# Optimization experiments

Measured on AMD Instinct MI355X. Metric: run time of the kernel, lower is better.

The kernel has to match this reference:

```python
import jax, jax.numpy as jnp
import numpy as np

N, E, H = 50000, 800000, 4
IN_C, HID, OUT = 256, 64, 64
NEG_SLOPE = 0.2   # PyG GATConv default leaky_relu slope
EPS_BN = 1e-5
EPS_SM = 1e-16    # PyG softmax denominator eps


def setup_inputs() -> dict:
    key = jax.random.key(0)
    ks = jax.random.split(key, 16)
    inp = {
        "x": jax.random.normal(ks[0], (N, IN_C), jnp.float32),
        "edge_index": jax.random.randint(ks[1], (2, E), 0, N, jnp.int32),
    }
    dims = [(IN_C, HID), (HID, HID), (HID, OUT)]
    j = 2
    for l, (di, do) in enumerate(dims):
        s = 1.0 / np.sqrt(di)
        inp[f"W{l}"] = jax.random.normal(ks[j], (di, H * do), jnp.float32) * s; j += 1
        inp[f"as{l}"] = jax.random.normal(ks[j], (H, do), jnp.float32) * 0.1; j += 1
        inp[f"ad{l}"] = jax.random.normal(ks[j], (H, do), jnp.float32) * 0.1; j += 1
        inp[f"b{l}"] = jnp.zeros((do,), jnp.float32)
    for l in range(2):  # BN after all but the last conv
        inp[f"g{l}"] = jnp.ones((HID,), jnp.float32)
        inp[f"be{l}"] = jnp.zeros((HID,), jnp.float32)
    return inp


def _gat_layer(x, src, dst, W, a_src, a_dst, bias):
    """PyG GATConv, heads=H, concat=False (mean over heads), add_self_loops already in src/dst."""
    n = x.shape[0]
    C = a_src.shape[1]
    h = (x @ W).reshape(n, H, C)                      # [N,H,C]
    a_l = jnp.einsum('nhc,hc->nh', h, a_src)          # src attention term per node
    a_r = jnp.einsum('nhc,hc->nh', h, a_dst)          # dst attention term per node
    e = jax.nn.leaky_relu(a_l[src] + a_r[dst], NEG_SLOPE)   # [E',H]
    # segment softmax over incoming edges of each dst node
    m = jax.ops.segment_max(e, dst, num_segments=n)
    m = jnp.where(jnp.isfinite(m), m, 0.0)
    p = jnp.exp(e - m[dst])
    den = jax.ops.segment_sum(p, dst, num_segments=n)
    alpha = p / (den[dst] + EPS_SM)                   # [E',H]
    msg = h[src] * alpha[:, :, None]                  # [E',H,C]
    out = jax.ops.segment_sum(msg, dst, num_segments=n)
    return out.mean(axis=1) + bias                    # concat=False -> head mean, then bias


def _bn(x, g, b):
    # BatchNorm1d training-mode statistics (biased variance), eps=1e-5
    mu = x.mean(axis=0)
    var = x.var(axis=0)
    return (x - mu) * jax.lax.rsqrt(var + EPS_BN) * g + b


def reference(x, edge_index, W0, as0, ad0, b0, W1, as1, ad1, b1,
              W2, as2, ad2, b2, g0, be0, g1, be1):
    n = x.shape[0]
    loops = jnp.arange(n, dtype=edge_index.dtype)
    src = jnp.concatenate([edge_index[0], loops])
    dst = jnp.concatenate([edge_index[1], loops])

    h = _gat_layer(x, src, dst, W0, as0, ad0, b0)
    h = jax.nn.relu(_bn(h, g0, be0))                  # dropout: eval mode (identity)
    h = _gat_layer(h, src, dst, W1, as1, ad1, b1)
    h = jax.nn.relu(_bn(h, g1, be1))
    out = _gat_layer(h, src, dst, W2, as2, ad2, b2)
    return out
```

## Files before the change

### kernel.cpp

```cpp
#include <hip/hip_runtime.h>
#include <hip/hip_fp16.h>
#include <math.h>

constexpr float NEG_SLOPE = 0.2f;
constexpr float EPS_BN = 1e-5f;
constexpr float EPS_SM = 1e-16f;

typedef _Float16 half8 __attribute__((ext_vector_type(8)));
typedef float f32x4 __attribute__((ext_vector_type(4)));

__device__ __forceinline__ float lrelu(float x){ return x >= 0.f ? x : NEG_SLOPE * x; }

typedef const __attribute__((address_space(1))) unsigned int* gas_u32;
typedef __attribute__((address_space(3))) unsigned int* las_u32;

__device__ __forceinline__ void llds16(const _Float16* g, _Float16* l){
  __builtin_amdgcn_global_load_lds((gas_u32)(const void*)g, (las_u32)(void*)l, 16, 0, 0);
}

__global__ void k_prep1(const float* __restrict__ x, _Float16* __restrict__ xh, int n8,
                        const int* __restrict__ ei, int E, int* __restrict__ cnt,
                        int* __restrict__ rank,
                        const float* __restrict__ W0, const float* __restrict__ W1,
                        const float* __restrict__ W2, _Float16* __restrict__ Wt0,
                        _Float16* __restrict__ Wt1, _Float16* __restrict__ Wt2,
                        float* __restrict__ bn, int* __restrict__ tick){
  int t = blockIdx.x * blockDim.x + threadIdx.x;
  if (t < n8){
    const float4* p = (const float4*)(x + (size_t)t * 8);
    float4 v0 = p[0], v1 = p[1];
    half8 h = {(_Float16)v0.x, (_Float16)v0.y, (_Float16)v0.z, (_Float16)v0.w,
               (_Float16)v1.x, (_Float16)v1.y, (_Float16)v1.z, (_Float16)v1.w};
    *(half8*)(xh + (size_t)t * 8) = h;
  }
  if (t < E) rank[t] = atomicAdd(&cnt[ei[E + t]], 1);
  if (t < 256) bn[t] = 0.f;
  if (t < 4) tick[t] = 0;
  if (t < 65536){
    int c = t & 255, k = t >> 8;
    Wt0[(size_t)c * 256 + k] = (_Float16)W0[(size_t)k * 256 + c];
  } else if (t < 81920){
    int u = t - 65536; int c = u & 255, k = u >> 8;
    Wt1[(size_t)c * 64 + k] = (_Float16)W1[(size_t)k * 256 + c];
  } else if (t < 98304){
    int u = t - 81920; int c = u & 255, k = u >> 8;
    Wt2[(size_t)c * 64 + k] = (_Float16)W2[(size_t)k * 256 + c];
  }
}

__global__ __launch_bounds__(256) void k_bsumscan(const int* __restrict__ cnt, int n, int chunk,
                                                  int* __restrict__ part, int* __restrict__ ptr,
                                                  int* __restrict__ tick){
  __shared__ int s[256];
  __shared__ int amLast;
  int b = blockIdx.x, t = threadIdx.x;
  int lo = b * chunk, hi = min(n, lo + chunk);
  int v = 0;
  for (int i = lo + t; i < hi; i += 256) v += cnt[i] + 1;
  s[t] = v;
  __syncthreads();
  #pragma unroll
  for (int off = 128; off > 0; off >>= 1){
    if (t < off) s[t] += s[t + off];
    __syncthreads();
  }
  if (t == 0) part[b] = s[0];
  __threadfence();
  if (t == 0) amLast = (atomicAdd(tick, 1) == (int)gridDim.x - 1) ? 1 : 0;
  __syncthreads();
  if (amLast){
    int pv = atomicAdd(&part[t], 0);
    s[t] = pv;
    __syncthreads();
    #pragma unroll
    for (int off = 1; off < 256; off <<= 1){
      int u = (t >= off) ? s[t - off] : 0;
      __syncthreads();
      s[t] += u;
      __syncthreads();
    }
    part[t] = s[t] - pv;
    if (t == 255) ptr[n] = s[255];
  }
}

__global__ __launch_bounds__(256) void k_localscan(const int* __restrict__ cnt, const int* __restrict__ part,
                                                   int n, int chunk, int* __restrict__ ptr,
                                                   int* __restrict__ csr_src){
  __shared__ int s[256];
  int b = blockIdx.x, t = threadIdx.x;
  int i = b * chunk + t;
  int c = (t < chunk && i < n) ? cnt[i] : 0;
  int v = (t < chunk && i < n) ? c + 1 : 0;
  s[t] = v;
  __syncthreads();
  #pragma unroll
  for (int off = 1; off < 256; off <<= 1){
    int u = (t >= off) ? s[t - off] : 0;
    __syncthreads();
    s[t] += u;
    __syncthreads();
  }
  if (t < chunk && i < n){
    int ex = part[b] + s[t] - v;
    ptr[i] = ex;
    csr_src[ex + c] = i;
  }
}

template<int LAYER>
__global__ __launch_bounds__(256, 2) void k_gemm(const _Float16* __restrict__ Xh,
    const float* __restrict__ Xf,
    const _Float16* __restrict__ Wt, const float* __restrict__ a_s, const float* __restrict__ a_d,
    __half* __restrict__ hb, float* __restrict__ al, float* __restrict__ ar, int nrows,
    const float* __restrict__ scale, const float* __restrict__ shift,
    const int* __restrict__ ei, int E, const int* __restrict__ rank,
    const int* __restrict__ rowptr, int* __restrict__ csr_src,
    int gemmBlocks, int N){
  constexpr int K = (LAYER == 0) ? 256 : 64;
  if (LAYER == 0 && (int)blockIdx.x >= gemmBlocks){
    int fb = (int)blockIdx.x - gemmBlocks;
    int xcd = (int)blockIdx.x & 7;
    int grp = fb >> 3;
    int ngrp = ((int)gridDim.x - gemmBlocks) >> 3;
    int nPer = N >> 3;
    int lo = xcd * nPer;
    int hi = (xcd == 7) ? N : lo + nPer;
    int stride = ngrp * 256;
    for (int e = grp * 256 + (int)threadIdx.x; e < E; e += stride){
      int dst = ei[E + e];
      if (dst >= lo && dst < hi)
        csr_src[rowptr[dst] + rank[e]] = ei[e];
    }
    return;
  }
  __shared__ _Float16 Alds[4][129][8];
  __shared__ _Float16 Blds[4][257][8];
  int tid = threadIdx.x;
  int m0 = blockIdx.x * 128;
  int w = tid >> 6, l = tid & 63;
  int lm = l & 15, lq = l >> 4;
  f32x4 acc[8][4] = {};

  for (int k0 = 0; k0 < K; k0 += 32){
    if (LAYER == 0){
      #pragma unroll
      for (int it = 0; it < 2; it++){
        int gr = m0 + it * 64 + l;
        if (gr < nrows)
          llds16(Xh + (size_t)gr * K + k0 + w * 8, &Alds[w][it * 64][0]);
      }
    } else {
      float4 sc0 = *(const float4*)(scale + k0 + w * 8);
      float4 sc1 = *(const float4*)(scale + k0 + w * 8 + 4);
      float4 sh0 = *(const float4*)(shift + k0 + w * 8);
      float4 sh1 = *(const float4*)(shift + k0 + w * 8 + 4);
      #pragma unroll
      for (int it = 0; it < 2; it++){
        int row = it * 64 + l;
        int gr = m0 + row;
        float4 v0 = make_float4(0,0,0,0), v1 = make_float4(0,0,0,0);
        if (gr < nrows){
          v0 = *(const float4*)(Xf + (size_t)gr * K + k0 + w * 8);
          v1 = *(const float4*)(Xf + (size_t)gr * K + k0 + w * 8 + 4);
        }
        v0.x = fmaxf(fmaf(v0.x, sc0.x, sh0.x), 0.f);
        v0.y = fmaxf(fmaf(v0.y, sc0.y, sh0.y), 0.f);
        v0.z = fmaxf(fmaf(v0.z, sc0.z, sh0.z), 0.f);
        v0.w = fmaxf(fmaf(v0.w, sc0.w, sh0.w), 0.f);
        v1.x = fmaxf(fmaf(v1.x, sc1.x, sh1.x), 0.f);
        v1.y = fmaxf(fmaf(v1.y, sc1.y, sh1.y), 0.f);
        v1.z = fmaxf(fmaf(v1.z, sc1.z, sh1.z), 0.f);
        v1.w = fmaxf(fmaf(v1.w, sc1.w, sh1.w), 0.f);
        half8 h = {(_Float16)v0.x, (_Float16)v0.y, (_Float16)v0.z, (_Float16)v0.w,
                   (_Float16)v1.x, (_Float16)v1.y, (_Float16)v1.z, (_Float16)v1.w};
        *(half8*)&Alds[w][row][0] = h;
      }
    }
    #pragma unroll
    for (int it = 0; it < 4; it++){
      int col = it * 64 + l;
      llds16(Wt + (size_t)col * K + k0 + w * 8, &Blds[w][it * 64][0]);
    }
    __syncthreads();
    half8 af[8];
    #pragma unroll
    for (int mf = 0; mf < 8; mf++) af[mf] = *(const half8*)&Alds[lq][mf * 16 + lm][0];
    #pragma unroll
    for (int j = 0; j < 4; j++){
      half8 bf = *(const half8*)&Blds[lq][(w * 4 + j) * 16 + lm][0];
      #pragma unroll
      for (int mf = 0; mf < 8; mf++)
        acc[mf][j] = __builtin_amdgcn_mfma_f32_16x16x32_f16(af[mf], bf, acc[mf][j], 0, 0, 0);
    }
    __syncthreads();
  }

  float asv[4], adv[4];
  #pragma unroll
  for (int j = 0; j < 4; j++){
    asv[j] = a_s[w * 64 + j * 16 + lm];
    adv[j] = a_d[w * 64 + j * 16 + lm];
  }
  #pragma unroll
  for (int mf = 0; mf < 8; mf++){
    #pragma unroll
    for (int reg = 0; reg < 4; reg++){
      float sl = acc[mf][0][reg] * asv[0] + acc[mf][1][reg] * asv[1]
               + acc[mf][2][reg] * asv[2] + acc[mf][3][reg] * asv[3];
      float sr = acc[mf][0][reg] * adv[0] + acc[mf][1][reg] * adv[1]
               + acc[mf][2][reg] * adv[2] + acc[mf][3][reg] * adv[3];
      #pragma unroll
      for (int off = 1; off < 16; off <<= 1){
        sl += __shfl_xor(sl, off);
        sr += __shfl_xor(sr, off);
      }
      int row = m0 + mf * 16 + lq * 4 + reg;
      if (lm == 0 && row < nrows){
        al[(size_t)row * 4 + w] = sl;
        ar[(size_t)row * 4 + w] = sr;
      }
      if (row < nrows){
        ushort4 pk;
        pk.x = __half_as_ushort(__float2half(acc[mf][0][reg]));
        pk.y = __half_as_ushort(__float2half(acc[mf][1][reg]));
        pk.z = __half_as_ushort(__float2half(acc[mf][2][reg]));
        pk.w = __half_as_ushort(__float2half(acc[mf][3][reg]));
        *(ushort4*)(hb + (size_t)row * 256 + w * 64 + lm * 4) = pk;
      }
    }
  }
}

#define AGG_STEP(QV, POFF) { \
    int je = j + (POFF) + eh; \
    float w = wbase[je * 4 + hd]; \
    int4 qq = QV; \
    int jn = je + 8; \
    if (jn < deg){ \
      int s = sbase[jn]; \
      QV = *(const int4*)((const char*)hb + (((unsigned)s << 9) + choff)); \
    } \
    const __half2* h2 = (const __half2*)&qq; \
    float2 f0 = __half22float2(h2[0]); \
    float2 f1 = __half22float2(h2[1]); \
    float2 f2 = __half22float2(h2[2]); \
    float2 f3 = __half22float2(h2[3]); \
    a0 = fmaf(f0.x, w, a0); a1 = fmaf(f0.y, w, a1); \
    a2 = fmaf(f1.x, w, a2); a3 = fmaf(f1.y, w, a3); \
    a4 = fmaf(f2.x, w, a4); a5 = fmaf(f2.y, w, a5); \
    a6 = fmaf(f3.x, w, a6); a7 = fmaf(f3.y, w, a7); \
  }

__global__ __launch_bounds__(256, 8) void k_node(const int* __restrict__ ptr,
    const int* __restrict__ csr, const __half* __restrict__ hb,
    const float* __restrict__ al, const float* __restrict__ ar,
    const float* __restrict__ bias, float* __restrict__ out, int N){
  __shared__ float4 wsm[4][64];
  __shared__ int    ssm[4][64];
  int n = (blockIdx.x * blockDim.x + threadIdx.x) >> 6;
  int lane = threadIdx.x & 63;
  int wv = threadIdx.x >> 6;
  if (n >= N) return;
  int beg = ptr[n], end = ptr[n + 1];
  int deg = end - beg;
  float4 arv = *(const float4*)(ar + (size_t)n * 4);

  if (deg <= 64){
    int idx = beg + lane;
    bool act = idx < end;
    int mye = act ? csr[idx] : 0;
    int eh = lane >> 5;
    int hd = (lane >> 3) & 3;
    int c8 = lane & 7;
    unsigned choff = (unsigned)(hd * 128 + c8 * 16);

    float e0 = -1e30f, e1 = -1e30f, e2 = -1e30f, e3 = -1e30f;
    if (act){
      float4 av = *(const float4*)((const char*)al + ((unsigned)mye << 4));
      e0 = lrelu(av.x + arv.x); e1 = lrelu(av.y + arv.y);
      e2 = lrelu(av.z + arv.z); e3 = lrelu(av.w + arv.w);
    }
    int s0 = __shfl(mye, 0 + eh), s1 = __shfl(mye, 2 + eh);
    int s2 = __shfl(mye, 4 + eh), s3 = __shfl(mye, 6 + eh);
    int4 q0 = *(const int4*)((const char*)hb + (((unsigned)s0 << 9) + choff));
    int4 q1 = *(const int4*)((const char*)hb + (((unsigned)s1 << 9) + choff));
    int4 q2 = *(const int4*)((const char*)hb + (((unsigned)s2 << 9) + choff));
    int4 q3 = *(const int4*)((const char*)hb + (((unsigned)s3 << 9) + choff));

    float m0 = e0, m1 = e1, m2 = e2, m3 = e3;
    #pragma unroll
    for (int off = 32; off > 0; off >>= 1){
      m0 = fmaxf(m0, __shfl_xor(m0, off));
      m1 = fmaxf(m1, __shfl_xor(m1, off));
      m2 = fmaxf(m2, __shfl_xor(m2, off));
      m3 = fmaxf(m3, __shfl_xor(m3, off));
    }
    float w0 = __expf(e0 - m0), w1 = __expf(e1 - m1);
    float w2 = __expf(e2 - m2), w3 = __expf(e3 - m3);
    float d0 = w0, d1 = w1, d2 = w2, d3 = w3;
    #pragma unroll
    for (int off = 32; off > 0; off >>= 1){
      d0 += __shfl_xor(d0, off);
      d1 += __shfl_xor(d1, off);
      d2 += __shfl_xor(d2, off);
      d3 += __shfl_xor(d3, off);
    }
    wsm[wv][lane] = make_float4(w0 / (d0 + EPS_SM), w1 / (d1 + EPS_SM),
                                w2 / (d2 + EPS_SM), w3 / (d3 + EPS_SM));
    ssm[wv][lane] = mye;
    __builtin_amdgcn_wave_barrier();

    const float* wbase = (const float*)&wsm[wv][0];
    const int*   sbase = &ssm[wv][0];
    float a0=0.f,a1=0.f,a2=0.f,a3=0.f,a4=0.f,a5=0.f,a6=0.f,a7=0.f;
    for (int j = 0; j < deg; j += 8){
      AGG_STEP(q0, 0)
      AGG_STEP(q1, 2)
      AGG_STEP(q2, 4)
      AGG_STEP(q3, 6)
    }
    #pragma unroll
    for (int off = 32; off >= 8; off >>= 1){
      a0 += __shfl_xor(a0, off); a1 += __shfl_xor(a1, off);
      a2 += __shfl_xor(a2, off); a3 += __shfl_xor(a3, off);
      a4 += __shfl_xor(a4, off); a5 += __shfl_xor(a5, off);
      a6 += __shfl_xor(a6, off); a7 += __shfl_xor(a7, off);
    }
    if (lane < 8){
      float* op = out + (size_t)n * 64 + c8 * 2;
      float2 b0 = *(const float2*)(bias + 0 * 16 + c8 * 2);
      float2 b1 = *(const float2*)(bias + 1 * 16 + c8 * 2);
      float2 b2 = *(const float2*)(bias + 2 * 16 + c8 * 2);
      float2 b3 = *(const float2*)(bias + 3 * 16 + c8 * 2);
      *(float2*)(op + 0)  = make_float2(a0 * 0.25f + b0.x, a4 * 0.25f + b0.y);
      *(float2*)(op + 16) = make_float2(a1 * 0.25f + b1.x, a5 * 0.25f + b1.y);
      *(float2*)(op + 32) = make_float2(a2 * 0.25f + b2.x, a6 * 0.25f + b2.y);
      *(float2*)(op + 48) = make_float2(a3 * 0.25f + b3.x, a7 * 0.25f + b3.y);
    }
  } else {
    int hd = lane >> 4;
    int t = lane & 15;
    const __half* hbase = hb + hd * 64 + t * 4;
    float ax = 0.f, ay = 0.f, az = 0.f, aw = 0.f;
    float m0 = -1e30f, m1 = -1e30f, m2 = -1e30f, m3 = -1e30f;
    for (int i = beg + lane; i < end; i += 64){
      int s = csr[i];
      float4 av = *(const float4*)(al + (size_t)s * 4);
      m0 = fmaxf(m0, lrelu(av.x + arv.x));
      m1 = fmaxf(m1, lrelu(av.y + arv.y));
      m2 = fmaxf(m2, lrelu(av.z + arv.z));
      m3 = fmaxf(m3, lrelu(av.w + arv.w));
    }
    #pragma unroll
    for (int off = 32; off > 0; off >>= 1){
      m0 = fmaxf(m0, __shfl_xor(m0, off));
      m1 = fmaxf(m1, __shfl_xor(m1, off));
      m2 = fmaxf(m2, __shfl_xor(m2, off));
      m3 = fmaxf(m3, __shfl_xor(m3, off));
    }
    float d0 = 0.f, d1 = 0.f, d2 = 0.f, d3 = 0.f;
    for (int i = beg + lane; i < end; i += 64){
      int s = csr[i];
      float4 av = *(const float4*)(al + (size_t)s * 4);
      d0 += __expf(lrelu(av.x + arv.x) - m0);
      d1 += __expf(lrelu(av.y + arv.y) - m1);
      d2 += __expf(lrelu(av.z + arv.z) - m2);
      d3 += __expf(lrelu(av.w + arv.w) - m3);
    }
    #pragma unroll
    for (int off = 32; off > 0; off >>= 1){
      d0 += __shfl_xor(d0, off);
      d1 += __shfl_xor(d1, off);
      d2 += __shfl_xor(d2, off);
      d3 += __shfl_xor(d3, off);
    }
    float i0 = 1.f / (d0 + EPS_SM), i1 = 1.f / (d1 + EPS_SM);
    float i2 = 1.f / (d2 + EPS_SM), i3 = 1.f / (d3 + EPS_SM);
    float arh = hd == 0 ? arv.x : hd == 1 ? arv.y : hd == 2 ? arv.z : arv.w;
    float mh  = hd == 0 ? m0 : hd == 1 ? m1 : hd == 2 ? m2 : m3;
    float ih  = hd == 0 ? i0 : hd == 1 ? i1 : hd == 2 ? i2 : i3;
    for (int i = beg; i < end; i++){
      int s = csr[i];
      float w = __expf(lrelu(al[(size_t)s * 4 + hd] + arh) - mh) * ih;
      ushort4 u = *(const ushort4*)(hbase + (size_t)s * 256);
      ax = fmaf(__half2float(__ushort_as_half(u.x)), w, ax);
      ay = fmaf(__half2float(__ushort_as_half(u.y)), w, ay);
      az = fmaf(__half2float(__ushort_as_half(u.z)), w, az);
      aw = fmaf(__half2float(__ushort_as_half(u.w)), w, aw);
    }
    #pragma unroll
    for (int off = 16; off <= 32; off <<= 1){
      ax += __shfl_xor(ax, off);
      ay += __shfl_xor(ay, off);
      az += __shfl_xor(az, off);
      aw += __shfl_xor(aw, off);
    }
    if (lane < 16){
      float* op = out + (size_t)n * 64;
      op[t]      = ax * 0.25f + bias[t];
      op[16 + t] = ay * 0.25f + bias[16 + t];
      op[32 + t] = az * 0.25f + bias[32 + t];
      op[48 + t] = aw * 0.25f + bias[48 + t];
    }
  }
}

__global__ __launch_bounds__(256) void k_bnstats(const float* __restrict__ x, int N,
                                                 float* __restrict__ gsum, float* __restrict__ gsq,
                                                 int* __restrict__ tick,
                                                 const float* __restrict__ g, const float* __restrict__ be,
                                                 float* __restrict__ scale, float* __restrict__ shift){
  int c = threadIdx.x & 63;
  int rg = threadIdx.x >> 6;
  float s = 0.f, q = 0.f;
  for (int r = blockIdx.x * 4 + rg; r < N; r += gridDim.x * 4){
    float v = x[(size_t)r * 64 + c];
    s += v; q += v * v;
  }
  __shared__ float ls[4][64], lq[4][64];
  __shared__ int amLast;
  ls[rg][c] = s; lq[rg][c] = q;
  __syncthreads();
  if (rg == 0){
    s = ls[0][c] + ls[1][c] + ls[2][c] + ls[3][c];
    q = lq[0][c] + lq[1][c] + lq[2][c] + lq[3][c];
    atomicAdd(&gsum[c], s);
    atomicAdd(&gsq[c], q);
  }
  __threadfence();
  if (threadIdx.x == 0)
    amLast = (atomicAdd(tick, 1) == (int)gridDim.x - 1) ? 1 : 0;
  __syncthreads();
  if (amLast && threadIdx.x < 64){
    float gs = atomicAdd(&gsum[c], 0.f);
    float gq = atomicAdd(&gsq[c], 0.f);
    float m = gs / (float)N;
    float v = gq / (float)N - m * m;
    float sc = g[c] * rsqrtf(v + EPS_BN);
    scale[c] = sc;
    shift[c] = be[c] - m * sc;
  }
}

extern "C" void kernel_launch(void* const* d_in, const int* in_sizes, int n_in,
                              void* d_out, int out_size, void* d_ws, size_t ws_size,
                              hipStream_t stream){
  const float* x  = (const float*)d_in[0];
  const int*   ei = (const int*)d_in[1];
  const float* W[3]  = {(const float*)d_in[2], (const float*)d_in[6],  (const float*)d_in[10]};
  const float* AS[3] = {(const float*)d_in[3], (const float*)d_in[7],  (const float*)d_in[11]};
  const float* AD[3] = {(const float*)d_in[4], (const float*)d_in[8],  (const float*)d_in[12]};
  const float* BI[3] = {(const float*)d_in[5], (const float*)d_in[9],  (const float*)d_in[13]};
  const float* G[2]  = {(const float*)d_in[14], (const float*)d_in[16]};
  const float* BE[2] = {(const float*)d_in[15], (const float*)d_in[17]};
  const int N = in_sizes[0] / 256;
  const int E = in_sizes[1] / 2;
  const int EN = E + N;

  char* wsb = (char*)d_ws;
  size_t off = 0;
  auto alloc = [&](size_t bytes) -> char* {
    char* p = wsb + off;
    off = (off + bytes + 255) & ~(size_t)255;
    return p;
  };
  int* cnt      = (int*)alloc((size_t)N * 4);
  int* rowptr   = (int*)alloc((size_t)(N + 1) * 4);
  int* part     = (int*)alloc(256 * 4);
  int* rank     = (int*)alloc((size_t)E * 4);
  int* csr      = (int*)alloc((size_t)EN * 4);
  _Float16* xh  = (_Float16*)alloc((size_t)N * 256 * 2);
  _Float16* Wt0 = (_Float16*)alloc((size_t)256 * 256 * 2);
  _Float16* Wt1 = (_Float16*)alloc((size_t)64 * 256 * 2);
  _Float16* Wt2 = (_Float16*)alloc((size_t)64 * 256 * 2);
  __half* hb    = (__half*)alloc((size_t)N * 256 * 2);
  float* al     = (float*)alloc((size_t)N * 4 * 4);
  float* ar     = (float*)alloc((size_t)N * 4 * 4);
  float* bufA   = (float*)alloc((size_t)N * 64 * 4);
  float* bn     = (float*)alloc(256 * 4);
  int*   tick   = (int*)alloc(4 * 4);
  float* murs   = (float*)alloc(128 * 4);

  const int chunk = (N + 255) / 256;
  const int n8 = N * 32;
  const int nodeGrid = (N + 3) / 4;

  hipMemsetAsync(cnt, 0, (size_t)N * 4, stream);
  k_prep1<<<(n8 + 255) / 256, 256, 0, stream>>>(x, xh, n8, ei, E, cnt, rank,
                                                W[0], W[1], W[2], Wt0, Wt1, Wt2, bn, tick);
  k_bsumscan<<<256, 256, 0, stream>>>(cnt, N, chunk, part, rowptr, tick + 2);
  k_localscan<<<256, 256, 0, stream>>>(cnt, part, N, chunk, rowptr, csr);

  int gemmGrid = (N + 127) / 128;
  const int FILLB = 1024;
  k_gemm<0><<<gemmGrid + FILLB, 256, 0, stream>>>(xh, nullptr, Wt0, AS[0], AD[0], hb, al, ar, N,
                                                  nullptr, nullptr, ei, E, rank, rowptr, csr,
                                                  gemmGrid, N);
  k_node<<<nodeGrid, 256, 0, stream>>>(rowptr, csr, hb, al, ar, BI[0], bufA, N);
  k_bnstats<<<256, 256, 0, stream>>>(bufA, N, bn, bn + 64, tick, G[0], BE[0], murs, murs + 64);
  k_gemm<1><<<gemmGrid, 256, 0, stream>>>(nullptr, bufA, Wt1, AS[1], AD[1], hb, al, ar, N,
                                          murs, murs + 64, nullptr, 0, nullptr, nullptr, nullptr,
                                          gemmGrid, N);
  k_node<<<nodeGrid, 256, 0, stream>>>(rowptr, csr, hb, al, ar, BI[1], bufA, N);
  k_bnstats<<<256, 256, 0, stream>>>(bufA, N, bn + 128, bn + 192, tick + 1, G[1], BE[1], murs, murs + 64);
  k_gemm<2><<<gemmGrid, 256, 0, stream>>>(nullptr, bufA, Wt2, AS[2], AD[2], hb, al, ar, N,
                                          murs, murs + 64, nullptr, 0, nullptr, nullptr, nullptr,
                                          gemmGrid, N);
  k_node<<<nodeGrid, 256, 0, stream>>>(rowptr, csr, hb, al, ar, BI[2], (float*)d_out, N);
}
```

Before: 531.6 us.

## Reorder layers 1-2 to aggregate input features before projecting through W

For layers 1 and 2, the linear projection is moved after aggregation: attention logits come from the input features dotted with precomputed W·a vectors. Each head's softmax-weighted sum of 64-wide fp16 inputs is gathered, then one GEMM with a head-stacked, 0.25-scaled weight applies projection, head mean and bias together. This cuts per-edge gather width from 256 to 64 halves per edge per head group and removes the per-layer 256-wide projection of all nodes. The cost is an extra small attention kernel, an N×256 fp16 intermediate, and different fp16 rounding order.

```diff
diff --git a/kernel.cpp b/kernel.cpp
--- a/kernel.cpp
+++ b/kernel.cpp
@@ -23,7 +23,10 @@
                         int* __restrict__ rank,
                         const float* __restrict__ W0, const float* __restrict__ W1,
                         const float* __restrict__ W2, _Float16* __restrict__ Wt0,
-                        _Float16* __restrict__ Wt1, _Float16* __restrict__ Wt2,
+                        _Float16* __restrict__ Wtp1, _Float16* __restrict__ Wtp2,
+                        const float* __restrict__ as1, const float* __restrict__ ad1,
+                        const float* __restrict__ as2, const float* __restrict__ ad2,
+                        float* __restrict__ va,
                         float* __restrict__ bn, int* __restrict__ tick){
   int t = blockIdx.x * blockDim.x + threadIdx.x;
   if (t < n8){
@@ -40,11 +43,24 @@
     int c = t & 255, k = t >> 8;
     Wt0[(size_t)c * 256 + k] = (_Float16)W0[(size_t)k * 256 + c];
   } else if (t < 81920){
-    int u = t - 65536; int c = u & 255, k = u >> 8;
-    Wt1[(size_t)c * 64 + k] = (_Float16)W1[(size_t)k * 256 + c];
+    int u = t - 65536; int c = u & 63, r = u >> 6;
+    Wtp1[(size_t)c * 256 + r] = (_Float16)(0.25f * W1[(size_t)(r & 63) * 256 + (r >> 6) * 64 + c]);
   } else if (t < 98304){
-    int u = t - 81920; int c = u & 255, k = u >> 8;
-    Wt2[(size_t)c * 64 + k] = (_Float16)W2[(size_t)k * 256 + c];
+    int u = t - 81920; int c = u & 63, r = u >> 6;
+    Wtp2[(size_t)c * 256 + r] = (_Float16)(0.25f * W2[(size_t)(r & 63) * 256 + (r >> 6) * 64 + c]);
+  } else if (t < 99328){
+    int u = t - 98304;
+    int layer = u >> 9;
+    int sd = (u >> 8) & 1;
+    int u2 = u & 255;
+    int c = u2 >> 2, h = u2 & 3;
+    const float* Wl = layer ? W2 : W1;
+    const float* av = layer ? (sd ? ad2 : as2) : (sd ? ad1 : as1);
+    float acc = 0.f;
+    #pragma unroll 4
+    for (int k = 0; k < 64; k++)
+      acc += Wl[(size_t)c * 256 + h * 64 + k] * av[h * 64 + k];
+    va[layer * 512 + c * 8 + sd * 4 + h] = acc;
   }
 }
 
@@ -110,14 +126,12 @@
 
 template<int LAYER>
 __global__ __launch_bounds__(256, 2) void k_gemm(const _Float16* __restrict__ Xh,
-    const float* __restrict__ Xf,
     const _Float16* __restrict__ Wt, const float* __restrict__ a_s, const float* __restrict__ a_d,
     __half* __restrict__ hb, float* __restrict__ al, float* __restrict__ ar, int nrows,
-    const float* __restrict__ scale, const float* __restrict__ shift,
     const int* __restrict__ ei, int E, const int* __restrict__ rank,
     const int* __restrict__ rowptr, int* __restrict__ csr_src,
     int gemmBlocks, int N){
-  constexpr int K = (LAYER == 0) ? 256 : 64;
+  constexpr int K = 256;
   if (LAYER == 0 && (int)blockIdx.x >= gemmBlocks){
     int fb = (int)blockIdx.x - gemmBlocks;
     int xcd = (int)blockIdx.x & 7;
@@ -143,39 +157,11 @@
   f32x4 acc[8][4] = {};
 
   for (int k0 = 0; k0 < K; k0 += 32){
-    if (LAYER == 0){
-      #pragma unroll
-      for (int it = 0; it < 2; it++){
-        int gr = m0 + it * 64 + l;
-        if (gr < nrows)
-          llds16(Xh + (size_t)gr * K + k0 + w * 8, &Alds[w][it * 64][0]);
-      }
-    } else {
-      float4 sc0 = *(const float4*)(scale + k0 + w * 8);
-      float4 sc1 = *(const float4*)(scale + k0 + w * 8 + 4);
-      float4 sh0 = *(const float4*)(shift + k0 + w * 8);
-      float4 sh1 = *(const float4*)(shift + k0 + w * 8 + 4);
-      #pragma unroll
-      for (int it = 0; it < 2; it++){
-        int row = it * 64 + l;
-        int gr = m0 + row;
-        float4 v0 = make_float4(0,0,0,0), v1 = make_float4(0,0,0,0);
-        if (gr < nrows){
-          v0 = *(const float4*)(Xf + (size_t)gr * K + k0 + w * 8);
-          v1 = *(const float4*)(Xf + (size_t)gr * K + k0 + w * 8 + 4);
-        }
-        v0.x = fmaxf(fmaf(v0.x, sc0.x, sh0.x), 0.f);
-        v0.y = fmaxf(fmaf(v0.y, sc0.y, sh0.y), 0.f);
-        v0.z = fmaxf(fmaf(v0.z, sc0.z, sh0.z), 0.f);
-        v0.w = fmaxf(fmaf(v0.w, sc0.w, sh0.w), 0.f);
-        v1.x = fmaxf(fmaf(v1.x, sc1.x, sh1.x), 0.f);
-        v1.y = fmaxf(fmaf(v1.y, sc1.y, sh1.y), 0.f);
-        v1.z = fmaxf(fmaf(v1.z, sc1.z, sh1.z), 0.f);
-        v1.w = fmaxf(fmaf(v1.w, sc1.w, sh1.w), 0.f);
-        half8 h = {(_Float16)v0.x, (_Float16)v0.y, (_Float16)v0.z, (_Float16)v0.w,
-                   (_Float16)v1.x, (_Float16)v1.y, (_Float16)v1.z, (_Float16)v1.w};
-        *(half8*)&Alds[w][row][0] = h;
-      }
+    #pragma unroll
+    for (int it = 0; it < 2; it++){
+      int gr = m0 + it * 64 + l;
+      if (gr < nrows)
+        llds16(Xh + (size_t)gr * K + k0 + w * 8, &Alds[w][it * 64][0]);
     }
     #pragma unroll
     for (int it = 0; it < 4; it++){
@@ -406,6 +392,268 @@
   }
 }
 
+__global__ __launch_bounds__(256) void k_attn(const float* __restrict__ bufA,
+    const float* __restrict__ scale, const float* __restrict__ shift,
+    const float* __restrict__ va,
+    _Float16* __restrict__ yh, float* __restrict__ al, float* __restrict__ ar, int N){
+  int n = (blockIdx.x * 256 + threadIdx.x) >> 4;
+  int t = threadIdx.x & 15;
+  if (n >= N) return;
+  float4 v  = *(const float4*)(bufA + (size_t)n * 64 + t * 4);
+  float4 sc = *(const float4*)(scale + t * 4);
+  float4 sh = *(const float4*)(shift + t * 4);
+  float y0 = fmaxf(fmaf(v.x, sc.x, sh.x), 0.f);
+  float y1 = fmaxf(fmaf(v.y, sc.y, sh.y), 0.f);
+  float y2 = fmaxf(fmaf(v.z, sc.z, sh.z), 0.f);
+  float y3 = fmaxf(fmaf(v.w, sc.w, sh.w), 0.f);
+  ushort4 pk;
+  pk.x = __half_as_ushort(__float2half(y0));
+  pk.y = __half_as_ushort(__float2half(y1));
+  pk.z = __half_as_ushort(__float2half(y2));
+  pk.w = __half_as_ushort(__float2half(y3));
+  *(ushort4*)(yh + (size_t)n * 64 + t * 4) = pk;
+
+  float p0=0,p1=0,p2=0,p3=0,p4=0,p5=0,p6=0,p7=0;
+  #define ATT_ACC(YV, J) { \
+    const float4 a = *(const float4*)(va + (t * 4 + (J)) * 8); \
+    const float4 b = *(const float4*)(va + (t * 4 + (J)) * 8 + 4); \
+    p0 = fmaf(YV, a.x, p0); p1 = fmaf(YV, a.y, p1); \
+    p2 = fmaf(YV, a.z, p2); p3 = fmaf(YV, a.w, p3); \
+    p4 = fmaf(YV, b.x, p4); p5 = fmaf(YV, b.y, p5); \
+    p6 = fmaf(YV, b.z, p6); p7 = fmaf(YV, b.w, p7); }
+  ATT_ACC(y0, 0) ATT_ACC(y1, 1) ATT_ACC(y2, 2) ATT_ACC(y3, 3)
+  #undef ATT_ACC
+  #pragma unroll
+  for (int off = 1; off < 16; off <<= 1){
+    p0 += __shfl_xor(p0, off); p1 += __shfl_xor(p1, off);
+    p2 += __shfl_xor(p2, off); p3 += __shfl_xor(p3, off);
+    p4 += __shfl_xor(p4, off); p5 += __shfl_xor(p5, off);
+    p6 += __shfl_xor(p6, off); p7 += __shfl_xor(p7, off);
+  }
+  if (t == 0){
+    *(float4*)(al + (size_t)n * 4) = make_float4(p0, p1, p2, p3);
+    *(float4*)(ar + (size_t)n * 4) = make_float4(p4, p5, p6, p7);
+  }
+}
+
+#define AGG_FMA(Q, W4) { \
+    union { uint2 u; __half2 h[2]; } _u; _u.u = (Q); \
+    float2 _fa = __half22float2(_u.h[0]); \
+    float2 _fb = __half22float2(_u.h[1]); \
+    a0.x = fmaf(_fa.x, (W4).x, a0.x); a0.y = fmaf(_fa.y, (W4).x, a0.y); \
+    a0.z = fmaf(_fb.x, (W4).x, a0.z); a0.w = fmaf(_fb.y, (W4).x, a0.w); \
+    a1.x = fmaf(_fa.x, (W4).y, a1.x); a1.y = fmaf(_fa.y, (W4).y, a1.y); \
+    a1.z = fmaf(_fb.x, (W4).y, a1.z); a1.w = fmaf(_fb.y, (W4).y, a1.w); \
+    a2.x = fmaf(_fa.x, (W4).z, a2.x); a2.y = fmaf(_fa.y, (W4).z, a2.y); \
+    a2.z = fmaf(_fb.x, (W4).z, a2.z); a2.w = fmaf(_fb.y, (W4).z, a2.w); \
+    a3.x = fmaf(_fa.x, (W4).w, a3.x); a3.y = fmaf(_fa.y, (W4).w, a3.y); \
+    a3.z = fmaf(_fb.x, (W4).w, a3.z); a3.w = fmaf(_fb.y, (W4).w, a3.w); \
+  }
+#define RED2(V) { V += __shfl_xor(V, 16); V += __shfl_xor(V, 32); }
+
+__global__ __launch_bounds__(256, 8) void k_agg(const int* __restrict__ ptr,
+    const int* __restrict__ csr, const _Float16* __restrict__ yh,
+    const float* __restrict__ al, const float* __restrict__ ar,
+    __half* __restrict__ aggh, int N){
+  __shared__ float4 wsm[4][64];
+  __shared__ int    ssm[4][64];
+  int n = (blockIdx.x * blockDim.x + threadIdx.x) >> 6;
+  int lane = threadIdx.x & 63;
+  int wv = threadIdx.x >> 6;
+  if (n >= N) return;
+  int beg = ptr[n], end = ptr[n + 1];
+  int deg = end - beg;
+  float4 arv = *(const float4*)(ar + (size_t)n * 4);
+  int eh = lane >> 4;
+  int t  = lane & 15;
+  float4 a0 = {0,0,0,0}, a1 = {0,0,0,0}, a2 = {0,0,0,0}, a3 = {0,0,0,0};
+
+  if (deg <= 64){
+    int idx = beg + lane;
+    bool act = idx < end;
+    int mye = act ? csr[idx] : 0;
+    float e0 = -1e30f, e1 = -1e30f, e2 = -1e30f, e3 = -1e30f;
+    if (act){
+      float4 av = *(const float4*)((const char*)al + ((unsigned)mye << 4));
+      e0 = lrelu(av.x + arv.x); e1 = lrelu(av.y + arv.y);
+      e2 = lrelu(av.z + arv.z); e3 = lrelu(av.w + arv.w);
+    }
+    int sA = __shfl(mye, eh);
+    uint2 qA = *(const uint2*)((const char*)yh + (((unsigned)sA) << 7) + t * 8);
+
+    float m0 = e0, m1 = e1, m2 = e2, m3 = e3;
+    #pragma unroll
+    for (int off = 32; off > 0; off >>= 1){
+      m0 = fmaxf(m0, __shfl_xor(m0, off));
+      m1 = fmaxf(m1, __shfl_xor(m1, off));
+      m2 = fmaxf(m2, __shfl_xor(m2, off));
+      m3 = fmaxf(m3, __shfl_xor(m3, off));
+    }
+    float w0 = __expf(e0 - m0), w1 = __expf(e1 - m1);
+    float w2 = __expf(e2 - m2), w3 = __expf(e3 - m3);
+    float d0 = w0, d1 = w1, d2 = w2, d3 = w3;
+    #pragma unroll
+    for (int off = 32; off > 0; off >>= 1){
+      d0 += __shfl_xor(d0, off);
+      d1 += __shfl_xor(d1, off);
+      d2 += __shfl_xor(d2, off);
+      d3 += __shfl_xor(d3, off);
+    }
+    wsm[wv][lane] = make_float4(w0 / (d0 + EPS_SM), w1 / (d1 + EPS_SM),
+                                w2 / (d2 + EPS_SM), w3 / (d3 + EPS_SM));
+    ssm[wv][lane] = mye;
+    __builtin_amdgcn_wave_barrier();
+
+    uint2 qB;
+    { int jb = min(4 + eh, 63);
+      int sB = ssm[wv][jb];
+      qB = *(const uint2*)((const char*)yh + (((unsigned)sB) << 7) + t * 8); }
+
+    for (int j = 0; j < deg; j += 8){
+      uint2 cur = qA;
+      { int ja = min(j + 8 + eh, 63);
+        int s2 = ssm[wv][ja];
+        qA = *(const uint2*)((const char*)yh + (((unsigned)s2) << 7) + t * 8); }
+      float4 w4 = wsm[wv][j + eh];
+      AGG_FMA(cur, w4)
+      uint2 curB = qB;
+      { int jb2 = min(j + 12 + eh, 63);
+        int s3 = ssm[wv][jb2];
+        qB = *(const uint2*)((const char*)yh + (((unsigned)s3) << 7) + t * 8); }
+      float4 w4b = wsm[wv][j + 4 + eh];
+      AGG_FMA(curB, w4b)
+    }
+  } else {
+    float m0 = -1e30f, m1 = -1e30f, m2 = -1e30f, m3 = -1e30f;
+    for (int i = beg + lane; i < end; i += 64){
+      int s = csr[i];
+      float4 av = *(const float4*)(al + (size_t)s * 4);
+      m0 = fmaxf(m0, lrelu(av.x + arv.x));
+      m1 = fmaxf(m1, lrelu(av.y + arv.y));
+      m2 = fmaxf(m2, lrelu(av.z + arv.z));
+      m3 = fmaxf(m3, lrelu(av.w + arv.w));
+    }
+    #pragma unroll
+    for (int off = 32; off > 0; off >>= 1){
+      m0 = fmaxf(m0, __shfl_xor(m0, off));
+      m1 = fmaxf(m1, __shfl_xor(m1, off));
+      m2 = fmaxf(m2, __shfl_xor(m2, off));
+      m3 = fmaxf(m3, __shfl_xor(m3, off));
+    }
+    float d0 = 0.f, d1 = 0.f, d2 = 0.f, d3 = 0.f;
+    for (int i = beg + lane; i < end; i += 64){
+      int s = csr[i];
+      float4 av = *(const float4*)(al + (size_t)s * 4);
+      d0 += __expf(lrelu(av.x + arv.x) - m0);
+      d1 += __expf(lrelu(av.y + arv.y) - m1);
+      d2 += __expf(lrelu(av.z + arv.z) - m2);
+      d3 += __expf(lrelu(av.w + arv.w) - m3);
+    }
+    #pragma unroll
+    for (int off = 32; off > 0; off >>= 1){
+      d0 += __shfl_xor(d0, off);
+      d1 += __shfl_xor(d1, off);
+      d2 += __shfl_xor(d2, off);
+      d3 += __shfl_xor(d3, off);
+    }
+    float i0 = 1.f / (d0 + EPS_SM), i1 = 1.f / (d1 + EPS_SM);
+    float i2 = 1.f / (d2 + EPS_SM), i3 = 1.f / (d3 + EPS_SM);
+    for (int i = beg; i < end; i += 4){
+      int ie = i + eh;
+      float w0 = 0.f, w1 = 0.f, w2 = 0.f, w3 = 0.f;
+      int s = 0;
+      if (ie < end){
+        s = csr[ie];
+        float4 av = *(const float4*)(al + (size_t)s * 4);
+        w0 = __expf(lrelu(av.x + arv.x) - m0) * i0;
+        w1 = __expf(lrelu(av.y + arv.y) - m1) * i1;
+        w2 = __expf(lrelu(av.z + arv.z) - m2) * i2;
+        w3 = __expf(lrelu(av.w + arv.w) - m3) * i3;
+      }
+      uint2 q = *(const uint2*)((const char*)yh + (((unsigned)s) << 7) + t * 8);
+      float4 w4 = make_float4(w0, w1, w2, w3);
+      AGG_FMA(q, w4)
+    }
+  }
+
+  RED2(a0.x) RED2(a0.y) RED2(a0.z) RED2(a0.w)
+  RED2(a1.x) RED2(a1.y) RED2(a1.z) RED2(a1.w)
+  RED2(a2.x) RED2(a2.y) RED2(a2.z) RED2(a2.w)
+  RED2(a3.x) RED2(a3.y) RED2(a3.z) RED2(a3.w)
+  if (eh == 0){
+    char* base = (char*)aggh + ((size_t)n << 9) + t * 8;
+    ushort4 pk;
+    pk.x = __half_as_ushort(__float2half(a0.x));
+    pk.y = __half_as_ushort(__float2half(a0.y));
+    pk.z = __half_as_ushort(__float2half(a0.z));
+    pk.w = __half_as_ushort(__float2half(a0.w));
+    *(ushort4*)(base + 0)   = pk;
+    pk.x = __half_as_ushort(__float2half(a1.x));
+    pk.y = __half_as_ushort(__float2half(a1.y));
+    pk.z = __half_as_ushort(__float2half(a1.z));
+    pk.w = __half_as_ushort(__float2half(a1.w));
+    *(ushort4*)(base + 128) = pk;
+    pk.x = __half_as_ushort(__float2half(a2.x));
+    pk.y = __half_as_ushort(__float2half(a2.y));
+    pk.z = __half_as_ushort(__float2half(a2.z));
+    pk.w = __half_as_ushort(__float2half(a2.w));
+    *(ushort4*)(base + 256) = pk;
+    pk.x = __half_as_ushort(__float2half(a3.x));
+    pk.y = __half_as_ushort(__float2half(a3.y));
+    pk.z = __half_as_ushort(__float2half(a3.z));
+    pk.w = __half_as_ushort(__float2half(a3.w));
+    *(ushort4*)(base + 384) = pk;
+  }
+}
+
+__global__ __launch_bounds__(256, 2) void k_gemmp(const _Float16* __restrict__ A,
+    const _Float16* __restrict__ Bt,
+    const float* __restrict__ bias, float* __restrict__ out, int nrows){
+  __shared__ _Float16 Alds[4][257][8];
+  __shared__ _Float16 Blds[4][65][8];
+  int tid = threadIdx.x;
+  int m0 = blockIdx.x * 256;
+  int w = tid >> 6, l = tid & 63;
+  int lm = l & 15, lq = l >> 4;
+  f32x4 acc[4][4] = {};
+  for (int k0 = 0; k0 < 256; k0 += 32){
+    #pragma unroll
+    for (int it = 0; it < 4; it++){
+      int gr = m0 + it * 64 + l;
+      if (gr < nrows)
+        llds16(A + (size_t)gr * 256 + k0 + w * 8, &Alds[w][it * 64][0]);
+    }
+    llds16(Bt + (size_t)l * 256 + k0 + w * 8, &Blds[w][0][0]);
+    __syncthreads();
+    half8 af[4];
+    #pragma unroll
+    for (int mf = 0; mf < 4; mf++) af[mf] = *(const half8*)&Alds[lq][w * 64 + mf * 16 + lm][0];
+    #pragma unroll
+    for (int j = 0; j < 4; j++){
+      half8 bf = *(const half8*)&Blds[lq][j * 16 + lm][0];
+      #pragma unroll
+      for (int mf = 0; mf < 4; mf++)
+        acc[mf][j] = __builtin_amdgcn_mfma_f32_16x16x32_f16(af[mf], bf, acc[mf][j], 0, 0, 0);
+    }
+    __syncthreads();
+  }
+  float bv[4];
+  #pragma unroll
+  for (int j = 0; j < 4; j++) bv[j] = bias[j * 16 + lm];
+  #pragma unroll
+  for (int mf = 0; mf < 4; mf++){
+    #pragma unroll
+    for (int reg = 0; reg < 4; reg++){
+      int row = m0 + w * 64 + mf * 16 + lq * 4 + reg;
+      if (row < nrows){
+        #pragma unroll
+        for (int j = 0; j < 4; j++)
+          out[(size_t)row * 64 + j * 16 + lm] = acc[mf][j][reg] + bv[j];
+      }
+    }
+  }
+}
+
 __global__ __launch_bounds__(256) void k_bnstats(const float* __restrict__ x, int N,
                                                  float* __restrict__ gsum, float* __restrict__ gsq,
                                                  int* __restrict__ tick,
@@ -472,12 +720,14 @@
   int* csr      = (int*)alloc((size_t)EN * 4);
   _Float16* xh  = (_Float16*)alloc((size_t)N * 256 * 2);
   _Float16* Wt0 = (_Float16*)alloc((size_t)256 * 256 * 2);
-  _Float16* Wt1 = (_Float16*)alloc((size_t)64 * 256 * 2);
-  _Float16* Wt2 = (_Float16*)alloc((size_t)64 * 256 * 2);
+  _Float16* Wtp1= (_Float16*)alloc((size_t)64 * 256 * 2);
+  _Float16* Wtp2= (_Float16*)alloc((size_t)64 * 256 * 2);
   __half* hb    = (__half*)alloc((size_t)N * 256 * 2);
   float* al     = (float*)alloc((size_t)N * 4 * 4);
   float* ar     = (float*)alloc((size_t)N * 4 * 4);
   float* bufA   = (float*)alloc((size_t)N * 64 * 4);
+  _Float16* yh  = (_Float16*)alloc((size_t)N * 64 * 2);
+  float* va     = (float*)alloc(1024 * 4);
   float* bn     = (float*)alloc(256 * 4);
   int*   tick   = (int*)alloc(4 * 4);
   float* murs   = (float*)alloc(128 * 4);
@@ -485,27 +735,27 @@
   const int chunk = (N + 255) / 256;
   const int n8 = N * 32;
   const int nodeGrid = (N + 3) / 4;
+  const int attnGrid = (N + 15) / 16;
+  const int gemmpGrid = (N + 255) / 256;
 
   hipMemsetAsync(cnt, 0, (size_t)N * 4, stream);
   k_prep1<<<(n8 + 255) / 256, 256, 0, stream>>>(x, xh, n8, ei, E, cnt, rank,
-                                                W[0], W[1], W[2], Wt0, Wt1, Wt2, bn, tick);
+                                                W[0], W[1], W[2], Wt0, Wtp1, Wtp2,
+                                                AS[1], AD[1], AS[2], AD[2], va, bn, tick);
   k_bsumscan<<<256, 256, 0, stream>>>(cnt, N, chunk, part, rowptr, tick + 2);
   k_localscan<<<256, 256, 0, stream>>>(cnt, part, N, chunk, rowptr, csr);
 
   int gemmGrid = (N + 127) / 128;
   const int FILLB = 1024;
-  k_gemm<0><<<gemmGrid + FILLB, 256, 0, stream>>>(xh, nullptr, Wt0, AS[0], AD[0], hb, al, ar, N,
-                                                  nullptr, nullptr, ei, E, rank, rowptr, csr,
-                                                  gemmGrid, N);
+  k_gemm<0><<<gemmGrid + FILLB, 256, 0, stream>>>(xh, Wt0, AS[0], AD[0], hb, al, ar, N,
+                                                  ei, E, rank, rowptr, csr, gemmGrid, N);
   k_node<<<nodeGrid, 256, 0, stream>>>(rowptr, csr, hb, al, ar, BI[0], bufA, N);
   k_bnstats<<<256, 256, 0, stream>>>(bufA, N, bn, bn + 64, tick, G[0], BE[0], murs, murs + 64);
-  k_gemm<1><<<gemmGrid, 256, 0, stream>>>(nullptr, bufA, Wt1, AS[1], AD[1], hb, al, ar, N,
-                                          murs, murs + 64, nullptr, 0, nullptr, nullptr, nullptr,
-                                          gemmGrid, N);
-  k_node<<<nodeGrid, 256, 0, stream>>>(rowptr, csr, hb, al, ar, BI[1], bufA, N);
+  k_attn<<<attnGrid, 256, 0, stream>>>(bufA, murs, murs + 64, va, yh, al, ar, N);
+  k_agg<<<nodeGrid, 256, 0, stream>>>(rowptr, csr, yh, al, ar, hb, N);
+  k_gemmp<<<gemmpGrid, 256, 0, stream>>>((const _Float16*)hb, Wtp1, BI[1], bufA, N);
   k_bnstats<<<256, 256, 0, stream>>>(bufA, N, bn + 128, bn + 192, tick + 1, G[1], BE[1], murs, murs + 64);
-  k_gemm<2><<<gemmGrid, 256, 0, stream>>>(nullptr, bufA, Wt2, AS[2], AD[2], hb, al, ar, N,
-                                          murs, murs + 64, nullptr, 0, nullptr, nullptr, nullptr,
-                                          gemmGrid, N);
-  k_node<<<nodeGrid, 256, 0, stream>>>(rowptr, csr, hb, al, ar, BI[2], (float*)d_out, N);
-}
+  k_attn<<<attnGrid, 256, 0, stream>>>(bufA, murs, murs + 64, va + 512, yh, al, ar, N);
+  k_agg<<<nodeGrid, 256, 0, stream>>>(rowptr, csr, yh, al, ar, hb, N);
+  k_gemmp<<<gemmpGrid, 256, 0, stream>>>((const _Float16*)hb, Wtp2, BI[2], (float*)d_out, N);
+}
```

After: 519.2 us. -2.3%, faster.
